# Performance work log

Measured on AMD Instinct MI355X. Metric: run time of the kernel, lower is better.

Reference implementation:

```python
import jax, jax.numpy as jnp
import numpy as np

K = 4096          # num_embeddings
D = 256           # embedding_dim
COMMIT = 0.25     # commitment_cost


def setup_inputs() -> dict:
    key = jax.random.key(0)
    k1, k2 = jax.random.split(key)
    z = jax.random.normal(k1, (16, D, 32, 32), dtype=jnp.float32)
    # codebook init: uniform(-1/K, 1/K) as in the torch module
    emb = jax.random.uniform(k2, (K, D), dtype=jnp.float32,
                             minval=-1.0 / K, maxval=1.0 / K)
    return {"z": z, "emb": emb}


def reference(z, emb):
    B, Dm, H, W = z.shape
    # (B, D, H, W) -> (B*H*W, D)
    z_flat = jnp.transpose(z, (0, 2, 3, 1)).reshape(-1, Dm)
    # squared L2 distances to every codebook vector: (N, K)
    distances = (jnp.sum(z_flat * z_flat, axis=1, keepdims=True)
                 + jnp.sum(emb * emb, axis=1)
                 - 2.0 * jnp.matmul(z_flat, emb.T))
    encoding_indices = jnp.argmin(distances, axis=1)            # (N,)
    encodings = jax.nn.one_hot(encoding_indices, emb.shape[0],
                               dtype=z.dtype)                   # (N, K)
    quantized = jnp.take(emb, encoding_indices, axis=0)         # == encodings @ emb

    sg = jax.lax.stop_gradient
    e_latent_loss = jnp.mean((sg(quantized) - z_flat) ** 2)
    q_latent_loss = jnp.mean((quantized - sg(z_flat)) ** 2)
    loss = q_latent_loss + COMMIT * e_latent_loss

    avg_probs = jnp.mean(encodings, axis=0)
    perplexity = jnp.exp(-jnp.sum(avg_probs * jnp.log(avg_probs + 1e-10)))

    # straight-through estimator
    quantized = z_flat + sg(quantized - z_flat)
    # NOTE: faithful to source: torch does .view(B, D, H, W) on the (N, D)
    # flat tensor WITHOUT permuting back -- a plain reshape, replicated here.
    quantized = quantized.reshape(B, Dm, H, W)
    return quantized, loss, perplexity, encodings
```

## Files before the change

kernel.cpp:

```cpp
#include <hip/hip_runtime.h>

#define NN 16384
#define KK 4096
#define DD 256

typedef __attribute__((ext_vector_type(8))) short short8;
typedef __attribute__((ext_vector_type(4))) float f32x4;

static __device__ __forceinline__ unsigned short f2bf(float f) {
  unsigned u = __float_as_uint(f);
  return (unsigned short)((u + 0x7FFFu + ((u >> 16) & 1u)) >> 16);
}

static __device__ __forceinline__ unsigned int mono(float f) {
  unsigned u = __float_as_uint(f);
  return (u & 0x80000000u) ? ~u : (u | 0x80000000u);
}

__global__ __launch_bounds__(256) void vq_prep_emb(
    const float* __restrict__ emb, unsigned short* __restrict__ eb,
    float* __restrict__ e2g) {
  const int wid = threadIdx.x >> 6, lane = threadIdx.x & 63;
  const int row = blockIdx.x * 4 + wid;
  float4 v = *reinterpret_cast<const float4*>(&emb[row * DD + lane * 4]);
  ushort4 w;
  w.x = f2bf(v.x); w.y = f2bf(v.y); w.z = f2bf(v.z); w.w = f2bf(v.w);
  *reinterpret_cast<ushort4*>(&eb[row * DD + lane * 4]) = w;
  float s = v.x * v.x + v.y * v.y + v.z * v.z + v.w * v.w;
  #pragma unroll
  for (int o = 1; o < 64; o <<= 1) s += __shfl_xor(s, o);
  if (lane == 0) e2g[row] = s;
}

__global__ __launch_bounds__(256) void vq_prep_z(
    const float* __restrict__ z, unsigned short* __restrict__ zb) {
  __shared__ unsigned short t[64][72];
  const int tid = threadIdx.x;
  const int bx = blockIdx.x;
  const int b = bx >> 6, rem = bx & 63, dt = rem >> 4, ht = rem & 15;
  const float* src = z + (long)b * 262144 + (long)dt * 64 * 1024 + ht * 64;
  #pragma unroll
  for (int p = 0; p < 16; ++p) {
    int idx = p * 256 + tid;
    int dl = idx >> 6, hl = idx & 63;
    t[hl][dl] = f2bf(src[dl * 1024 + hl]);
  }
  __syncthreads();
  unsigned short* dst = zb + ((long)b * 1024 + (long)ht * 64) * DD + dt * 64;
  #pragma unroll
  for (int p = 0; p < 2; ++p) {
    int idx = p * 256 + tid;
    int hl = idx >> 3, c8 = idx & 7;
    short8 v = *reinterpret_cast<const short8*>(&t[hl][c8 * 8]);
    *reinterpret_cast<short8*>(&dst[(long)hl * DD + c8 * 8]) = v;
  }
}

__global__ __launch_bounds__(256) void vq_gemm(
    const unsigned short* __restrict__ eb, const unsigned short* __restrict__ zb,
    const float* __restrict__ e2g, unsigned long long* __restrict__ keys) {
  __shared__ unsigned short At[128 * 64];
  __shared__ unsigned short Bt[128 * 64];
  __shared__ float e2s[128];
  __shared__ unsigned long long wkey[2][128];

  const int tid = threadIdx.x;
  const int bm = blockIdx.x;
  const int bn = blockIdx.y;
  const int lane = tid & 63, wid = tid >> 6;
  const int wm = wid >> 1, wn = wid & 1;
  const int l16 = lane & 15, g4 = lane >> 4;

  if (tid < 128) {
    e2s[tid] = e2g[bm * 128 + tid];
    wkey[0][tid] = ~0ull;
    wkey[1][tid] = ~0ull;
  }

  const long abase = (long)bm * 128 * DD;
  const long bbase = (long)bn * 128 * DD;

  f32x4 acc[4][4];
  #pragma unroll
  for (int mi = 0; mi < 4; ++mi)
    #pragma unroll
    for (int ni = 0; ni < 4; ++ni) acc[mi][ni] = (f32x4){0.f, 0.f, 0.f, 0.f};

  for (int kt = 0; kt < 4; ++kt) {
    __syncthreads();
    {
      const int lr = lane >> 3, lc = (lane & 7) * 8;
      #pragma unroll
      for (int c = 0; c < 4; ++c) {
        const int row0 = wid * 32 + c * 8;
        const unsigned short* ga =
            eb + abase + (long)(row0 + lr) * DD + kt * 64 + lc;
        __builtin_amdgcn_global_load_lds(
            (const __attribute__((address_space(1))) void*)ga,
            (__attribute__((address_space(3))) void*)&At[row0 * 64], 16, 0, 0);
        const unsigned short* gb =
            zb + bbase + (long)(row0 + lr) * DD + kt * 64 + lc;
        __builtin_amdgcn_global_load_lds(
            (const __attribute__((address_space(1))) void*)gb,
            (__attribute__((address_space(3))) void*)&Bt[row0 * 64], 16, 0, 0);
      }
    }
    __syncthreads();

    #pragma unroll
    for (int kk = 0; kk < 2; ++kk) {
      short8 a[4], b[4];
      #pragma unroll
      for (int mi = 0; mi < 4; ++mi)
        a[mi] = *reinterpret_cast<const short8*>(
            &At[(wm * 64 + mi * 16 + l16) * 64 + kk * 32 + g4 * 8]);
      #pragma unroll
      for (int ni = 0; ni < 4; ++ni)
        b[ni] = *reinterpret_cast<const short8*>(
            &Bt[(wn * 64 + ni * 16 + l16) * 64 + kk * 32 + g4 * 8]);
      #pragma unroll
      for (int mi = 0; mi < 4; ++mi)
        #pragma unroll
        for (int ni = 0; ni < 4; ++ni)
          acc[mi][ni] = __builtin_amdgcn_mfma_f32_16x16x32_bf16(
              a[mi], b[ni], acc[mi][ni], 0, 0, 0);
    }
  }

  #pragma unroll
  for (int ni = 0; ni < 4; ++ni) {
    float bv = INFINITY;
    int bi = 0;
    #pragma unroll
    for (int mi = 0; mi < 4; ++mi) {
      #pragma unroll
      for (int r = 0; r < 4; ++r) {
        int krow = wm * 64 + mi * 16 + g4 * 4 + r;
        float s = fmaf(-2.0f, acc[mi][ni][r], e2s[krow]);
        if (s < bv) { bv = s; bi = bm * 128 + krow; }
      }
    }
    unsigned long long key =
        ((unsigned long long)mono(bv) << 32) | (unsigned)bi;
    unsigned long long o;
    o = __shfl_xor(key, 16); if (o < key) key = o;
    o = __shfl_xor(key, 32); if (o < key) key = o;
    if (g4 == 0) wkey[wm][wn * 64 + ni * 16 + l16] = key;
  }
  __syncthreads();
  if (tid < 128) {
    unsigned long long k0 = wkey[0][tid], k1 = wkey[1][tid];
    atomicMin(&keys[(long)bn * 128 + tid], k0 < k1 ? k0 : k1);
  }
}

__global__ __launch_bounds__(256) void vq_finish(
    const float* __restrict__ z, const float* __restrict__ emb,
    const unsigned long long* __restrict__ keys, unsigned int* __restrict__ counts,
    float* __restrict__ lossacc, float* __restrict__ outq, float* __restrict__ enc) {
  __shared__ float ztile[64][257];
  __shared__ int sidx[64];
  __shared__ float wsum[4];

  const int tid = threadIdx.x;
  const int n0 = blockIdx.x * 64;
  const long zbase = (long)(n0 >> 10) * 262144 + (long)(n0 & 1023);

  {
    int n4 = (tid & 15) << 2;
    int dl = tid >> 4;
    for (int p = 0; p < 16; ++p) {
      int d = p * 16 + dl;
      float4 v = *reinterpret_cast<const float4*>(&z[zbase + (long)d * 1024 + n4]);
      ztile[n4 + 0][d] = v.x;
      ztile[n4 + 1][d] = v.y;
      ztile[n4 + 2][d] = v.z;
      ztile[n4 + 3][d] = v.w;
    }
  }
  if (tid < 64) {
    int n = n0 + tid;
    int idx = (int)(keys[n] & 0xFFFFFFFFULL);
    sidx[tid] = idx;
    atomicAdd(&counts[idx], 1u);
    enc[(long)n * KK + idx] = 1.0f;
  }
  __syncthreads();

  float lacc = 0.f;
  const int d = tid;
  for (int nl = 0; nl < 64; ++nl) {
    int idx = sidx[nl];
    float e = emb[idx * DD + d];
    float zz = ztile[nl][d];
    float df = e - zz;
    lacc += df * df;
    outq[(long)(n0 + nl) * DD + d] = zz + (e - zz);
  }
  #pragma unroll
  for (int o = 1; o < 64; o <<= 1) lacc += __shfl_xor(lacc, o);
  if ((tid & 63) == 0) wsum[tid >> 6] = lacc;
  __syncthreads();
  if (tid == 0) atomicAdd(lossacc, wsum[0] + wsum[1] + wsum[2] + wsum[3]);
}

__global__ void vq_scalars(const unsigned int* __restrict__ counts,
                           const float* __restrict__ lossacc,
                           float* __restrict__ outs) {
  __shared__ double sh[256];
  int t = threadIdx.x;
  double ent = 0.0;
  for (int k = t; k < KK; k += 256) {
    double p = (double)counts[k] / (double)NN;
    ent += p * log(p + 1e-10);
  }
  sh[t] = ent;
  __syncthreads();
  for (int s = 128; s > 0; s >>= 1) {
    if (t < s) sh[t] += sh[t + s];
    __syncthreads();
  }
  if (t == 0) {
    outs[0] = lossacc[0] * 1.25f / ((float)NN * (float)DD);
    outs[1] = (float)exp(-sh[0]);
  }
}

extern "C" void kernel_launch(void* const* d_in, const int* in_sizes, int n_in,
                              void* d_out, int out_size, void* d_ws, size_t ws_size,
                              hipStream_t stream) {
  const float* z = (const float*)d_in[0];
  const float* emb = (const float*)d_in[1];
  float* out = (float*)d_out;
  float* outq = out;
  float* outs = out + 4194304;
  float* enc = out + 4194306;

  char* ws = (char*)d_ws;
  unsigned short* zb = (unsigned short*)ws;
  unsigned short* eb = (unsigned short*)(ws + 8388608);
  float* e2g = (float*)(ws + 10485760);
  unsigned long long* keys = (unsigned long long*)(ws + 10502144);
  unsigned int* counts = (unsigned int*)(ws + 10633216);
  float* lossacc = (float*)(ws + 10649600);

  hipMemsetAsync(keys, 0xFF, 131072, stream);
  hipMemsetAsync(ws + 10633216, 0, 16388, stream);
  hipMemsetAsync(enc, 0, (size_t)NN * KK * 4, stream);

  vq_prep_emb<<<1024, 256, 0, stream>>>(emb, eb, e2g);
  vq_prep_z<<<1024, 256, 0, stream>>>(z, zb);
  vq_gemm<<<dim3(32, 128), 256, 0, stream>>>(eb, zb, e2g, keys);
  vq_finish<<<NN / 64, 256, 0, stream>>>(z, emb, keys, counts, lossacc, outq, enc);
  vq_scalars<<<1, 256, 0, stream>>>(counts, lossacc, outs);
}
```

Baseline: 396.4 us.

## Fuse prep kernels and memsets; zero encodings inside GEMM epilogue

Merges the codebook and latent prep kernels plus the key/count/loss initialization into one launch, replacing three hipMemsetAsync calls. The 256MB one-hot encoding buffer is now zeroed by each GEMM block after its compute, so the write traffic can overlap with MFMA work from other blocks instead of running as a separate memset. This removes launch overhead but adds heavy store traffic to the GEMM kernel, which may contend with its loads.

Result: faster. 352.5 us (-11.1%).

```diff
diff --git a/kernel.cpp b/kernel.cpp
--- a/kernel.cpp
+++ b/kernel.cpp
@@ -17,48 +17,58 @@
   return (u & 0x80000000u) ? ~u : (u | 0x80000000u);
 }
 
-__global__ __launch_bounds__(256) void vq_prep_emb(
-    const float* __restrict__ emb, unsigned short* __restrict__ eb,
-    float* __restrict__ e2g) {
-  const int wid = threadIdx.x >> 6, lane = threadIdx.x & 63;
-  const int row = blockIdx.x * 4 + wid;
-  float4 v = *reinterpret_cast<const float4*>(&emb[row * DD + lane * 4]);
-  ushort4 w;
-  w.x = f2bf(v.x); w.y = f2bf(v.y); w.z = f2bf(v.z); w.w = f2bf(v.w);
-  *reinterpret_cast<ushort4*>(&eb[row * DD + lane * 4]) = w;
-  float s = v.x * v.x + v.y * v.y + v.z * v.z + v.w * v.w;
-  #pragma unroll
-  for (int o = 1; o < 64; o <<= 1) s += __shfl_xor(s, o);
-  if (lane == 0) e2g[row] = s;
-}
-
-__global__ __launch_bounds__(256) void vq_prep_z(
-    const float* __restrict__ z, unsigned short* __restrict__ zb) {
+__global__ __launch_bounds__(256) void vq_prep(
+    const float* __restrict__ z, const float* __restrict__ emb,
+    unsigned short* __restrict__ zb, unsigned short* __restrict__ eb,
+    float* __restrict__ e2g, unsigned long long* __restrict__ keys,
+    unsigned int* __restrict__ counts, float* __restrict__ lossacc) {
   __shared__ unsigned short t[64][72];
   const int tid = threadIdx.x;
   const int bx = blockIdx.x;
-  const int b = bx >> 6, rem = bx & 63, dt = rem >> 4, ht = rem & 15;
-  const float* src = z + (long)b * 262144 + (long)dt * 64 * 1024 + ht * 64;
-  #pragma unroll
-  for (int p = 0; p < 16; ++p) {
-    int idx = p * 256 + tid;
-    int dl = idx >> 6, hl = idx & 63;
-    t[hl][dl] = f2bf(src[dl * 1024 + hl]);
-  }
-  __syncthreads();
-  unsigned short* dst = zb + ((long)b * 1024 + (long)ht * 64) * DD + dt * 64;
-  #pragma unroll
-  for (int p = 0; p < 2; ++p) {
-    int idx = p * 256 + tid;
-    int hl = idx >> 3, c8 = idx & 7;
-    short8 v = *reinterpret_cast<const short8*>(&t[hl][c8 * 8]);
-    *reinterpret_cast<short8*>(&dst[(long)hl * DD + c8 * 8]) = v;
+
+  if (bx < 1024) {
+    const int b = bx >> 6, rem = bx & 63, dt = rem >> 4, ht = rem & 15;
+    const float* src = z + (long)b * 262144 + (long)dt * 65536 + ht * 64;
+    #pragma unroll
+    for (int p = 0; p < 16; ++p) {
+      int idx = p * 256 + tid;
+      int dl = idx >> 6, hl = idx & 63;
+      t[hl][dl] = f2bf(src[dl * 1024 + hl]);
+    }
+    __syncthreads();
+    unsigned short* dst = zb + ((long)b * 1024 + (long)ht * 64) * DD + dt * 64;
+    #pragma unroll
+    for (int p = 0; p < 2; ++p) {
+      int idx = p * 256 + tid;
+      int hl = idx >> 3, c8 = idx & 7;
+      short8 v = *reinterpret_cast<const short8*>(&t[hl][c8 * 8]);
+      *reinterpret_cast<short8*>(&dst[(long)hl * DD + c8 * 8]) = v;
+    }
+  } else if (bx < 2048) {
+    const int wid = tid >> 6, lane = tid & 63;
+    const int row = (bx - 1024) * 4 + wid;
+    float4 v = *reinterpret_cast<const float4*>(&emb[row * DD + lane * 4]);
+    ushort4 w;
+    w.x = f2bf(v.x); w.y = f2bf(v.y); w.z = f2bf(v.z); w.w = f2bf(v.w);
+    *reinterpret_cast<ushort4*>(&eb[row * DD + lane * 4]) = w;
+    float s = v.x * v.x + v.y * v.y + v.z * v.z + v.w * v.w;
+    #pragma unroll
+    for (int o = 1; o < 64; o <<= 1) s += __shfl_xor(s, o);
+    if (lane == 0) e2g[row] = s;
+  } else {
+    int tt = (bx - 2048) * 256 + tid;
+    #pragma unroll
+    for (int i = 0; i < 8; ++i) keys[tt * 8 + i] = ~0ull;
+    counts[tt * 2] = 0u;
+    counts[tt * 2 + 1] = 0u;
+    if (tt == 0) lossacc[0] = 0.f;
   }
 }
 
 __global__ __launch_bounds__(256) void vq_gemm(
     const unsigned short* __restrict__ eb, const unsigned short* __restrict__ zb,
-    const float* __restrict__ e2g, unsigned long long* __restrict__ keys) {
+    const float* __restrict__ e2g, unsigned long long* __restrict__ keys,
+    float* __restrict__ enc) {
   __shared__ unsigned short At[128 * 64];
   __shared__ unsigned short Bt[128 * 64];
   __shared__ float e2s[128];
@@ -152,6 +162,14 @@
     unsigned long long k0 = wkey[0][tid], k1 = wkey[1][tid];
     atomicMin(&keys[(long)bn * 128 + tid], k0 < k1 ? k0 : k1);
   }
+
+  {
+    const long base = ((long)(bm * 128 + bn)) * 16384;
+    const f32x4 zero4 = (f32x4){0.f, 0.f, 0.f, 0.f};
+    #pragma unroll
+    for (int i = 0; i < 16; ++i)
+      *reinterpret_cast<f32x4*>(&enc[base + (long)(i * 256 + tid) * 4]) = zero4;
+  }
 }
 
 __global__ __launch_bounds__(256) void vq_finish(
@@ -244,13 +262,8 @@
   unsigned int* counts = (unsigned int*)(ws + 10633216);
   float* lossacc = (float*)(ws + 10649600);
 
-  hipMemsetAsync(keys, 0xFF, 131072, stream);
-  hipMemsetAsync(ws + 10633216, 0, 16388, stream);
-  hipMemsetAsync(enc, 0, (size_t)NN * KK * 4, stream);
-
-  vq_prep_emb<<<1024, 256, 0, stream>>>(emb, eb, e2g);
-  vq_prep_z<<<1024, 256, 0, stream>>>(z, zb);
-  vq_gemm<<<dim3(32, 128), 256, 0, stream>>>(eb, zb, e2g, keys);
+  vq_prep<<<2056, 256, 0, stream>>>(z, emb, zb, eb, e2g, keys, counts, lossacc);
+  vq_gemm<<<dim3(32, 128), 256, 0, stream>>>(eb, zb, e2g, keys, enc);
   vq_finish<<<NN / 64, 256, 0, stream>>>(z, emb, keys, counts, lossacc, outq, enc);
   vq_scalars<<<1, 256, 0, stream>>>(counts, lossacc, outs);
 }
```
